# Performance work log

Hardware: AMD Instinct MI355X
Metric: run time of the kernel (lower is better)

Reference implementation:

```python
import jax, jax.numpy as jnp
import numpy as np

B, L, C, P_LEN = 512, 336, 321, 96
WIN, HID = 12, 25
PRED_SEG = P_LEN // WIN


def setup_inputs() -> dict:
    key = jax.random.key(0)
    ks = jax.random.split(key, 8)
    s = 1.0 / np.sqrt(HID)
    u = lambda k, shape: jax.random.uniform(k, shape, minval=-s, maxval=s, dtype=jnp.float32)
    return {
        "x": jax.random.normal(ks[0], (B, L, C), dtype=jnp.float32),
        "segmentor": jax.random.uniform(ks[1], (C, WIN, 1), dtype=jnp.float32),  # torch.rand init
        "W_ih": u(ks[2], (C, 4 * HID, 1)),
        "W_hh": u(ks[3], (C, 4 * HID, HID)),
        "b_ih": u(ks[4], (C, 4 * HID)),
        "b_hh": u(ks[5], (C, 4 * HID)),
        "Wp": u(ks[6], (C, 1, HID)),
        "bp": u(ks[7], (C, 1)),
        "pred_seg": PRED_SEG,
    }


def reference(x, segmentor, W_ih, W_hh, b_ih, b_hh, Wp, bp, pred_seg):
    b_, l_, c_ = x.shape
    w_ = segmentor.shape[1]
    s_ = l_ // w_
    h_ = W_hh.shape[-1]

    seq_mean = jnp.mean(x, axis=1, keepdims=True)            # [B,1,C]
    xc = jnp.transpose(x - seq_mean, (0, 2, 1))              # [B,C,L]
    seg2d = segmentor[..., 0]                                # [C,W]
    # segment embedding: [B,C,S,W] @ [C,W] -> time-major [S,B,C]
    seg_in = jnp.einsum('bcsw,cw->sbc', xc.reshape(b_, c_, s_, w_), seg2d)

    Wx = W_ih[:, :, 0]                                       # [C,4H]
    bias = b_ih + b_hh                                       # [C,4H]

    def cell(h, c, xt):  # xt [B,C]; h,c [B,C,H]; torch gate order i,f,g,o
        gates = xt[..., None] * Wx[None] + jnp.einsum('bch,cgh->bcg', h, W_hh) + bias[None]
        i, f, g, o = jnp.split(gates, 4, axis=-1)
        c_new = jax.nn.sigmoid(f) * c + jax.nn.sigmoid(i) * jnp.tanh(g)
        h_new = jax.nn.sigmoid(o) * jnp.tanh(c_new)
        return h_new, c_new

    h0 = jnp.zeros((b_, c_, h_), x.dtype)
    c0 = jnp.zeros_like(h0)

    def enc(carry, xt):
        h, c = carry
        h, c = cell(h, c, xt)
        return (h, c), None

    (h, c), _ = jax.lax.scan(enc, (h0, c0), seg_in)

    def proj(h):  # [B,C,H] -> [B,C]
        return jnp.einsum('bch,ch->bc', h, Wp[:, 0, :]) + bp[:, 0][None]

    out0 = proj(h)

    def dec(carry, _):
        h, c, inp = carry
        h, c = cell(h, c, inp)
        out = proj(h)
        return (h, c, out), out

    _, rest = jax.lax.scan(dec, (h, c, out0), None, length=pred_seg - 1)
    preds = jnp.concatenate([out0[None], rest], axis=0)      # [P,B,C]
    preds = jnp.transpose(preds, (1, 2, 0))                  # [B,C,P]
    # de-segment: [B,C,P] x [C,W] -> [B,C,P*W]
    y = jnp.einsum('bcp,cw->bcpw', preds, seg2d).reshape(b_, c_, pred_seg * w_)
    return jnp.transpose(y, (0, 2, 1)) + seq_mean
```

## Files before the change

### kernel.cpp

```cpp
#include <hip/hip_runtime.h>
#include <math.h>

#define NB 512
#define NL 336
#define NC 321
#define NS 28
#define NW 12
#define NH 25
#define NP 8
#define NG 100
#define NT (NS + NP - 1)
#define BSL 16
#define WPB 4
#define LOG2E 1.44269504088896340736f
#define N2LOG2E -2.88539008177792681472f

typedef __attribute__((ext_vector_type(8))) _Float16 f16x8;
typedef __attribute__((ext_vector_type(4))) float f32x4;

union F8 { f16x8 v; _Float16 h[8]; };

__device__ __forceinline__ void set_q3f(F8& b, bool q3, float xt) {
    b.h[1] = q3 ? (_Float16)xt : b.h[1];
    b.h[2] = q3 ? (_Float16)1.0f : b.h[2];
    b.h[3] = q3 ? (_Float16)0.0f : b.h[3];
    b.h[4] = q3 ? (_Float16)0.0f : b.h[4];
    b.h[5] = q3 ? (_Float16)0.0f : b.h[5];
    b.h[6] = q3 ? (_Float16)0.0f : b.h[6];
    b.h[7] = q3 ? (_Float16)0.0f : b.h[7];
}

extern "C" __global__ __launch_bounds__(384)
void k_seg(const float* __restrict__ x, const float* __restrict__ seg,
           float* __restrict__ seg_inT, float* __restrict__ meanw) {
    const int b = blockIdx.x;
    const int c = threadIdx.x;
    if (c >= NC) return;
    float sw[NW];
#pragma unroll
    for (int w = 0; w < NW; ++w) sw[w] = seg[c * NW + w];
    float acc[NS];
    float sum = 0.0f;
    const float* xb = x + (size_t)b * NL * NC + c;
#pragma unroll 1
    for (int s = 0; s < NS; ++s) {
        float a = 0.0f;
#pragma unroll
        for (int w = 0; w < NW; ++w) {
            float v = xb[(s * NW + w) * NC];
            sum += v;
            a = fmaf(v, sw[w], a);
        }
        acc[s] = a;
    }
    const float mean = sum * (1.0f / (float)NL);
    float ssum = 0.0f;
#pragma unroll
    for (int w = 0; w < NW; ++w) ssum += sw[w];
    meanw[b * NC + c] = mean;
#pragma unroll
    for (int s = 0; s < NS; ++s)
        seg_inT[((size_t)s * NC + c) * NB + b] = acc[s] - mean * ssum;
}

extern "C" __global__ __launch_bounds__(256, 4)
void k_lstm(const float* __restrict__ seg_inT, const float* __restrict__ W_ih,
            const float* __restrict__ W_hh, const float* __restrict__ b_ih,
            const float* __restrict__ b_hh, const float* __restrict__ Wp,
            const float* __restrict__ bp, float* __restrict__ preds) {
    const int c = blockIdx.x;
    const int wv = threadIdx.x >> 6;
    const int lane = threadIdx.x & 63;
    const int b0 = (blockIdx.y * WPB + wv) * BSL;
    const int bb = lane & 15;
    const int q  = lane >> 4;
    const bool q3 = (q == 3);

    const int qq = bb >> 2, rr = bb & 3;
    const float srow = (rr == 2) ? 2.88539008177792681472f : LOG2E;
    const float* __restrict__ whh = W_hh + (size_t)c * NG * NH;
    const float* __restrict__ wxp = W_ih + (size_t)c * NG;
    const float* __restrict__ bip = b_ih + (size_t)c * NG;
    const float* __restrict__ bhp = b_hh + (size_t)c * NG;
    F8 afr[8];
#pragma unroll 1
    for (int mg = 0; mg < 8; ++mg) {
        const int jj = qq * 8 + mg;
        const int grow = rr * NH + jj;
        F8 f0;
#pragma unroll
        for (int e = 0; e < 8; ++e) {
            const int k = q * 8 + e;
            float v0 = 0.0f;
            if (jj < NH) {
                if (k < NH)         v0 = whh[grow * NH + k] * srow;
                else if (k == 25)   v0 = wxp[grow] * srow;
                else if (k == 26)   v0 = (bip[grow] + bhp[grow]) * srow;
            }
            f0.h[e] = (_Float16)v0;
        }
        afr[mg] = f0;
    }

    float wpl[8];
#pragma unroll
    for (int mg = 0; mg < 8; ++mg) {
        const int j = q * 8 + mg;
        wpl[mg] = (j < NH) ? Wp[(size_t)c * NH + j] : 0.0f;
    }
    const float bpc = bp[c];

    F8 ph;
    {
        const float x0 = seg_inT[(size_t)c * NB + b0 + bb];
#pragma unroll
        for (int e = 0; e < 8; ++e) ph.h[e] = (_Float16)0.0f;
        set_q3f(ph, q3, x0);
    }

    float cst[8];
#pragma unroll
    for (int mg = 0; mg < 8; ++mg) cst[mg] = 0.0f;

#pragma unroll 1
    for (int t = 0; t < NT; ++t) {
        const bool enc_next = (t + 1 < NS);
        const bool do_proj = (t >= NS - 1);
        const bool have_next = (t + 1 < NT);

        float xn = 0.0f;
        if (enc_next)
            xn = seg_inT[((size_t)(t + 1) * NC + c) * NB + b0 + bb];

        f32x4 av[8];
#pragma unroll
        for (int mg = 0; mg < 8; ++mg) {
            f32x4 z = {0.0f, 0.0f, 0.0f, 0.0f};
            av[mg] = __builtin_amdgcn_mfma_f32_16x16x32_f16(afr[mg].v, ph.v, z, 0, 0, 0);
        }

        float ei[8], ef[8], eg[8], eo[8];
#pragma unroll
        for (int mg = 0; mg < 8; ++mg) {
            ei[mg] = __builtin_amdgcn_exp2f(-av[mg][0]);
            ef[mg] = __builtin_amdgcn_exp2f(-av[mg][1]);
            eg[mg] = __builtin_amdgcn_exp2f(-av[mg][2]);
            eo[mg] = __builtin_amdgcn_exp2f(-av[mg][3]);
        }

        float hnv[8];
        float pp = 0.0f;
#pragma unroll
        for (int mg = 0; mg < 8; ++mg) {
            const float p1f = 1.0f + ef[mg];
            const float pig = (1.0f + ei[mg]) * (1.0f + eg[mg]);
            const float num = fmaf(cst[mg], pig, (1.0f - eg[mg]) * p1f);
            const float cn  = num * __builtin_amdgcn_rcpf(p1f * pig);
            const float et  = __builtin_amdgcn_exp2f(cn * N2LOG2E);
            const float hn  = (1.0f - et) *
                              __builtin_amdgcn_rcpf((1.0f + eo[mg]) * (1.0f + et));
            cst[mg] = cn;
            hnv[mg] = hn;
            if (do_proj) pp = fmaf(hn, wpl[mg], pp);
        }

        float ov = 0.0f;
        if (do_proj) {
            pp += __shfl_xor(pp, 16);
            pp += __shfl_xor(pp, 32);
            ov = pp + bpc;
            if (q == 0)
                preds[((size_t)c * NP + (t - (NS - 1))) * NB + b0 + bb] = ov;
        }

        if (have_next) {
#pragma unroll
            for (int e = 0; e < 8; ++e) ph.h[e] = (_Float16)hnv[e];
            set_q3f(ph, q3, enc_next ? xn : ov);
        }
    }
}

extern "C" __global__ __launch_bounds__(384)
void k_out(const float* __restrict__ preds, const float* __restrict__ seg,
           const float* __restrict__ meanw, float* __restrict__ out) {
    const int b = blockIdx.x;
    const int c = threadIdx.x;
    if (c >= NC) return;
    float sw[NW];
#pragma unroll
    for (int w = 0; w < NW; ++w) sw[w] = seg[c * NW + w];
    const float mean = meanw[b * NC + c];
    float pv[NP];
#pragma unroll
    for (int p = 0; p < NP; ++p) pv[p] = preds[((size_t)c * NP + p) * NB + b];
    float* ob = out + (size_t)b * (NP * NW) * NC + c;
#pragma unroll
    for (int p = 0; p < NP; ++p) {
#pragma unroll
        for (int w = 0; w < NW; ++w) {
            ob[(p * NW + w) * NC] = fmaf(pv[p], sw[w], mean);
        }
    }
}

extern "C" void kernel_launch(void* const* d_in, const int* in_sizes, int n_in,
                              void* d_out, int out_size, void* d_ws, size_t ws_size,
                              hipStream_t stream) {
    const float* x    = (const float*)d_in[0];
    const float* seg  = (const float*)d_in[1];
    const float* W_ih = (const float*)d_in[2];
    const float* W_hh = (const float*)d_in[3];
    const float* b_ih = (const float*)d_in[4];
    const float* b_hh = (const float*)d_in[5];
    const float* Wp   = (const float*)d_in[6];
    const float* bp   = (const float*)d_in[7];
    float* out = (float*)d_out;

    float* seg_inT = (float*)d_ws;
    float* meanw   = seg_inT + (size_t)NS * NC * NB;
    float* preds   = meanw + (size_t)NB * NC;

    k_seg<<<NB, 384, 0, stream>>>(x, seg, seg_inT, meanw);
    k_lstm<<<dim3(NC, NB / (BSL * WPB)), 256, 0, stream>>>(
        seg_inT, W_ih, W_hh, b_ih, b_hh, Wp, bp, preds);
    k_out<<<NB, 384, 0, stream>>>(preds, seg, meanw, out);
}
```

Baseline: 332.6 us.

## Unroll segment reduction, split output kernel over predictions, use Newton reciprocals

```diff
diff --git a/kernel.cpp b/kernel.cpp
--- a/kernel.cpp
+++ b/kernel.cpp
@@ -20,6 +20,16 @@
 
 union F8 { f16x8 v; _Float16 h[8]; };
 
+__device__ __forceinline__ float frcp3(float x) {
+    union { float f; unsigned u; } v; v.f = x;
+    v.u = 0x7EF311C3u - v.u;
+    float r = v.f;
+    r = r * fmaf(-x, r, 2.0f);
+    r = r * fmaf(-x, r, 2.0f);
+    r = r * fmaf(-x, r, 2.0f);
+    return r;
+}
+
 __device__ __forceinline__ void set_q3f(F8& b, bool q3, float xt) {
     b.h[1] = q3 ? (_Float16)xt : b.h[1];
     b.h[2] = q3 ? (_Float16)1.0f : b.h[2];
@@ -40,20 +50,28 @@
 #pragma unroll
     for (int w = 0; w < NW; ++w) sw[w] = seg[c * NW + w];
     float acc[NS];
-    float sum = 0.0f;
+    float sum0 = 0.0f, sum1 = 0.0f, sum2 = 0.0f, sum3 = 0.0f;
     const float* xb = x + (size_t)b * NL * NC + c;
-#pragma unroll 1
+#pragma unroll
     for (int s = 0; s < NS; ++s) {
         float a = 0.0f;
-#pragma unroll
-        for (int w = 0; w < NW; ++w) {
-            float v = xb[(s * NW + w) * NC];
-            sum += v;
-            a = fmaf(v, sw[w], a);
-        }
+        float t0 = 0.0f, t1 = 0.0f, t2 = 0.0f, t3 = 0.0f;
+#pragma unroll
+        for (int w = 0; w < NW; w += 4) {
+            const float v0 = xb[(s * NW + w) * NC];
+            const float v1 = xb[(s * NW + w + 1) * NC];
+            const float v2 = xb[(s * NW + w + 2) * NC];
+            const float v3 = xb[(s * NW + w + 3) * NC];
+            t0 += v0; t1 += v1; t2 += v2; t3 += v3;
+            a = fmaf(v0, sw[w], a);
+            a = fmaf(v1, sw[w + 1], a);
+            a = fmaf(v2, sw[w + 2], a);
+            a = fmaf(v3, sw[w + 3], a);
+        }
+        sum0 += t0; sum1 += t1; sum2 += t2; sum3 += t3;
         acc[s] = a;
     }
-    const float mean = sum * (1.0f / (float)NL);
+    const float mean = ((sum0 + sum1) + (sum2 + sum3)) * (1.0f / (float)NL);
     float ssum = 0.0f;
 #pragma unroll
     for (int w = 0; w < NW; ++w) ssum += sw[w];
@@ -155,10 +173,9 @@
             const float p1f = 1.0f + ef[mg];
             const float pig = (1.0f + ei[mg]) * (1.0f + eg[mg]);
             const float num = fmaf(cst[mg], pig, (1.0f - eg[mg]) * p1f);
-            const float cn  = num * __builtin_amdgcn_rcpf(p1f * pig);
+            const float cn  = num * frcp3(p1f * pig);
             const float et  = __builtin_amdgcn_exp2f(cn * N2LOG2E);
-            const float hn  = (1.0f - et) *
-                              __builtin_amdgcn_rcpf((1.0f + eo[mg]) * (1.0f + et));
+            const float hn  = (1.0f - et) * frcp3((1.0f + eo[mg]) * (1.0f + et));
             cst[mg] = cn;
             hnv[mg] = hn;
             if (do_proj) pp = fmaf(hn, wpl[mg], pp);
@@ -185,23 +202,15 @@
 void k_out(const float* __restrict__ preds, const float* __restrict__ seg,
            const float* __restrict__ meanw, float* __restrict__ out) {
     const int b = blockIdx.x;
+    const int p = blockIdx.y;
     const int c = threadIdx.x;
     if (c >= NC) return;
-    float sw[NW];
-#pragma unroll
-    for (int w = 0; w < NW; ++w) sw[w] = seg[c * NW + w];
+    const float pv = preds[((size_t)c * NP + p) * NB + b];
     const float mean = meanw[b * NC + c];
-    float pv[NP];
-#pragma unroll
-    for (int p = 0; p < NP; ++p) pv[p] = preds[((size_t)c * NP + p) * NB + b];
-    float* ob = out + (size_t)b * (NP * NW) * NC + c;
-#pragma unroll
-    for (int p = 0; p < NP; ++p) {
-#pragma unroll
-        for (int w = 0; w < NW; ++w) {
-            ob[(p * NW + w) * NC] = fmaf(pv[p], sw[w], mean);
-        }
-    }
+    float* ob = out + ((size_t)b * (NP * NW) + p * NW) * NC + c;
+#pragma unroll
+    for (int w = 0; w < NW; ++w)
+        ob[w * NC] = fmaf(pv, seg[c * NW + w], mean);
 }
 
 extern "C" void kernel_launch(void* const* d_in, const int* in_sizes, int n_in,
@@ -224,5 +233,5 @@
     k_seg<<<NB, 384, 0, stream>>>(x, seg, seg_inT, meanw);
     k_lstm<<<dim3(NC, NB / (BSL * WPB)), 256, 0, stream>>>(
         seg_inT, W_ih, W_hh, b_ih, b_hh, Wp, bp, preds);
-    k_out<<<NB, 384, 0, stream>>>(preds, seg, meanw, out);
-}
+    k_out<<<dim3(NB, NP), 384, 0, stream>>>(preds, seg, meanw, out);
+}
```

New measurement: 369.0 us. +10.9%, slower.
